# Kernel tuning notes

Measured on AMD Instinct MI355X. Metric: run time of the kernel, lower is better.

Reference implementation:

```python
import jax, jax.numpy as jnp
import numpy as np
import math

NEG_INF = -1e9
B, S, P, HID, NH, DH = 2, 1024, 128, 1024, 16, 64
NUM_SEG = 2


def setup_inputs() -> dict:
    key = jax.random.key(0)
    ks = jax.random.split(key, 16)
    f32 = jnp.float32
    inp = {
        'content_stream': jax.random.normal(ks[0], (B, S, HID), f32),
        'query_stream': jax.random.normal(ks[1], (B, P, HID), f32),
        'positional_encoding': jax.random.normal(ks[2], (B, 2 * S, HID), f32),
        'segment_matrix': jax.random.randint(ks[3], (B, S, S), 0, 2) > 0,
        'segment_encoding': jax.random.normal(ks[4], (NUM_SEG, NH, DH), f32) * 0.02,
        'segment_bias': jax.random.normal(ks[5], (NH, DH), f32) * 0.02,
        'content_mask': (jax.random.uniform(ks[6], (B, 1, S, S)) < 0.1).astype(f32),
        'query_mask': (jax.random.uniform(ks[7], (B, 1, S, S)) < 0.1).astype(f32),
        'target_mapping': jax.nn.one_hot(jax.random.randint(ks[8], (B, P), 0, S), S, dtype=f32),
        'content_bias': jax.random.normal(ks[9], (NH, DH), f32) * 0.02,
        'position_bias': jax.random.normal(ks[10], (NH, DH), f32) * 0.02,
        # projection params (no bias, XLNet-style split/merge projections)
        'wq': jax.random.normal(ks[11], (HID, NH, DH), f32) * 0.02,
        'wkc': jax.random.normal(ks[12], (HID, NH, DH), f32) * 0.02,
        'wv': jax.random.normal(ks[13], (HID, NH, DH), f32) * 0.02,
        'wkp': jax.random.normal(ks[14], (HID, NH, DH), f32) * 0.02,
        'wo': jax.random.normal(ks[15], (NH, DH, HID), f32) * 0.02,
    }
    return inp


def _rel_shift(x, klen):
    # x: [B, H, Q, R]; TransformerXL pad/reshape/slice relative shift, then keep cols 1:1+klen
    b, h, q, r = x.shape
    padded = jnp.pad(x, ((0, 0), (0, 0), (0, 0), (1, 0)))
    shifted = padded.reshape(b, h, r + 1, q)[:, :, 1:].reshape(b, h, q, r)
    return shifted[..., 1:1 + klen]


def _attention(q, kc, v, kp, content_bias, position_bias,
               segment_matrix, segment_encoding, segment_bias, token_mask):
    # q,kc,v: [B,S,H,D]; kp: [B,2S,H,D]
    content = jnp.einsum('bqhd,brhd->bhqr', q + content_bias, kc)          # [B,H,S,S]
    position = jnp.einsum('bqhd,brhd->bhqr', q + position_bias, kp)        # [B,H,S,2S]
    position = _rel_shift(position, content.shape[-1])                     # [B,H,S,S]
    segment = jnp.einsum('bqhd,shd->bhqs', q + segment_bias, segment_encoding)  # [B,H,S,2]
    segment = jnp.where(segment_matrix[:, None], segment[..., 1:], segment[..., :1])  # [B,H,S,S]
    scores = (content + position + segment) * (1.0 / math.sqrt(DH))
    scores = scores + token_mask * NEG_INF
    weights = jax.nn.softmax(scores, axis=-1)  # dropout is identity at inference
    return jnp.einsum('bhqr,brhd->bqhd', weights, v)


def reference(content_stream, query_stream, positional_encoding, segment_matrix,
              segment_encoding, segment_bias, content_mask, query_mask,
              target_mapping, content_bias, position_bias,
              wq, wkc, wv, wkp, wo):
    split = lambda x, w: jnp.einsum('bth,hnd->btnd', x, w)
    # state is None -> keys/values come from content_stream only
    q = split(content_stream, wq)
    kc = split(content_stream, wkc)
    v = split(content_stream, wv)
    kp = split(positional_encoding, wkp)

    content_out = _attention(q, kc, v, kp, content_bias, position_bias,
                             segment_matrix, segment_encoding, segment_bias, content_mask)
    content_output = jnp.einsum('bqnd,ndh->bqh', content_out, wo)

    qg = split(query_stream, wq)                                   # [B,P,H,D]
    qg = jnp.einsum('bphd,bpq->bqhd', qg, target_mapping)          # scatter to [B,S,H,D]
    query_out = _attention(qg, kc, v, kp, content_bias, position_bias,
                           segment_matrix, segment_encoding, segment_bias, query_mask)
    query_out = jnp.einsum('bqhd,bpq->bphd', query_out, target_mapping)  # gather back to [B,P,H,D]
    query_output = jnp.einsum('bpnd,ndh->bph', query_out, wo)

    return content_output, query_output
```

## Files before the change

### kernel.cpp

```cpp
#include <hip/hip_runtime.h>
#include <math.h>


static constexpr int Bc  = 2;
static constexpr int Sc  = 1024;
static constexpr int Pc  = 128;
static constexpr int HIDc = 1024;
static constexpr int NHc = 16;
static constexpr int DHc = 64;

typedef __bf16 bf16;
typedef __bf16 bf16x8 __attribute__((ext_vector_type(8)));
typedef float  f32x4  __attribute__((ext_vector_type(4)));

#define MFMA16(a, b, c) __builtin_amdgcn_mfma_f32_16x16x32_bf16((a), (b), (c), 0, 0, 0)

__global__ void sniff_seg(const unsigned char* __restrict__ seg, int* __restrict__ flag) {
    const int t = threadIdx.x;
    int nz1 = 0, nz23 = 0;
    for (int i = t * 64; i < t * 64 + 64; ++i) {
        unsigned char c = seg[i];
        int m = i & 3;
        if (m == 1 && c) nz1 = 1;
        if ((m == 2 || m == 3) && c) nz23 = 1;
    }
    nz1 = __any(nz1);
    nz23 = __any(nz23);
    if (t == 0) flag[0] = nz1 ? 0 : (nz23 ? 2 : 1);
}

__global__ void bits3(const void* __restrict__ seg, const int* __restrict__ flag,
                      const float* __restrict__ cm, const float* __restrict__ qm,
                      unsigned* __restrict__ segb, unsigned* __restrict__ cmb,
                      unsigned* __restrict__ qmb) {
    const int bid = blockIdx.x;
    const int which = bid >> 8;
    const int idx = (bid & 255) * 256 + threadIdx.x;
    unsigned wv = 0;
    if (which == 0) {
        const int mode = flag[0];
        if (mode == 0) {
            const unsigned char* s = (const unsigned char*)seg + (size_t)idx * 32;
#pragma unroll
            for (int k = 0; k < 32; ++k) wv |= (s[k] != 0) ? (1u << k) : 0u;
        } else if (mode == 1) {
            const int* s = (const int*)seg + (size_t)idx * 32;
#pragma unroll
            for (int k = 0; k < 32; ++k) wv |= (s[k] != 0) ? (1u << k) : 0u;
        } else {
            const float* s = (const float*)seg + (size_t)idx * 32;
#pragma unroll
            for (int k = 0; k < 32; ++k) wv |= (s[k] != 0.f) ? (1u << k) : 0u;
        }
        segb[idx] = wv;
    } else {
        const float* s = (which == 1 ? cm : qm) + (size_t)idx * 32;
#pragma unroll
        for (int k = 0; k < 32; ++k) wv |= (s[k] != 0.f) ? (1u << k) : 0u;
        (which == 1 ? cmb : qmb)[idx] = wv;
    }
}

__global__ __launch_bounds__(256) void prep_split(
        const float* __restrict__ content, const float* __restrict__ posenc,
        const float* __restrict__ querys,
        const float* __restrict__ wq, const float* __restrict__ wkc,
        const float* __restrict__ wvp, const float* __restrict__ wkp,
        const float* __restrict__ wo,
        bf16* __restrict__ ch, bf16* __restrict__ ph, bf16* __restrict__ qh,
        bf16* __restrict__ wqkvh, bf16* __restrict__ wqkvl,
        bf16* __restrict__ wkphh, bf16* __restrict__ wkpll,
        bf16* __restrict__ woh, bf16* __restrict__ wol) {
    __shared__ float tile[32][33];
    const int bid = blockIdx.x;
    if (bid < 3200) {
        const float* src; bf16* hdst; size_t base;
        if (bid < 1024)      { src = content; hdst = ch; base = (size_t)bid * 2048; }
        else if (bid < 3072) { src = posenc;  hdst = ph; base = (size_t)(bid - 1024) * 2048; }
        else                 { src = querys;  hdst = qh; base = (size_t)(bid - 3072) * 2048; }
        const size_t i = base + (size_t)threadIdx.x * 8;
        float xs[8];
        *(float4*)xs       = *(const float4*)(src + i);
        *(float4*)(xs + 4) = *(const float4*)(src + i + 4);
        union { bf16 b[8]; uint4 u; } H;
#pragma unroll
        for (int k = 0; k < 8; ++k) H.b[k] = (bf16)xs[k];
        *(uint4*)(hdst + i) = H.u;
        return;
    }
    const int wid = bid - 3200;
    const int z = wid >> 10, rem = wid & 1023;
    const float* W = z == 0 ? wq : z == 1 ? wkc : z == 2 ? wvp : z == 3 ? wkp : wo;
    bf16* Th = z < 3 ? wqkvh + (size_t)z * HIDc * HIDc : (z == 3 ? wkphh : woh);
    bf16* Tl = z < 3 ? wqkvl + (size_t)z * HIDc * HIDc : (z == 3 ? wkpll : wol);
    const int k0 = (rem >> 5) * 32, n0 = (rem & 31) * 32;
    const int c = threadIdx.x & 31, r0 = threadIdx.x >> 5;
#pragma unroll
    for (int rr = 0; rr < 4; ++rr) {
        int r = r0 + rr * 8;
        tile[r][c] = W[(size_t)(k0 + r) * HIDc + n0 + c];
    }
    __syncthreads();
#pragma unroll
    for (int rr = 0; rr < 4; ++rr) {
        int n = r0 + rr * 8;
        float x = tile[c][n];
        bf16 hb = (bf16)x;
        Th[(size_t)(n0 + n) * HIDc + k0 + c] = hb;
        Tl[(size_t)(n0 + n) * HIDc + k0 + c] = (bf16)(x - (float)hb);
    }
}

__global__ __launch_bounds__(256) void big_gemm(
        const bf16* __restrict__ conth, const bf16* __restrict__ posh,
        const bf16* __restrict__ quh,
        const bf16* __restrict__ wqkvh, const bf16* __restrict__ wqkvl,
        const bf16* __restrict__ wkph, const bf16* __restrict__ wkpl,
        float* __restrict__ qf, bf16* __restrict__ kch,
        bf16* __restrict__ vtg, bf16* __restrict__ kpho,
        float* __restrict__ qgf) {
    __shared__ bf16 AhS[128][40], BhS[128][40], BlS[128][40];
    const int bid = blockIdx.x;
    const int vb = (bid & 7) * 82 + (bid >> 3);
    int mode, bx, by;
    const bf16 *Ahp, *Bhp, *Blp;
    if (vb < 384)      { mode = 1; bx = vb >> 4; by = vb & 15;
                          Ahp = conth; Bhp = wqkvh; Blp = wqkvl; }
    else if (vb < 640) { mode = 2; int r = vb - 384; bx = r >> 5; by = r & 31;
                          Ahp = posh;  Bhp = wkph;  Blp = wkpl; }
    else               { mode = 0; int r = vb - 640; bx = r & 7; by = r >> 3;
                          Ahp = quh;   Bhp = wqkvh; Blp = wqkvl; }
    const int t = threadIdx.x, lane = t & 63, wv = t >> 6;
    const int g = lane >> 4, ml = lane & 15;
    const int m0 = by * 128, n0 = bx * 128;
    const int moff = (wv & 1) * 64, noff = (wv >> 1) * 64;
    const int row2 = t >> 1, c16 = (t & 1) * 16;
    const int K = HIDc;

    f32x4 acc[4][4];
#pragma unroll
    for (int i = 0; i < 4; ++i)
#pragma unroll
        for (int j = 0; j < 4; ++j) acc[i][j] = (f32x4){0.f, 0.f, 0.f, 0.f};

    uint4 rah0, rah1, rbh0, rbh1, rbl0, rbl1;
    auto gload = [&](int k0) {
        size_t ab = (size_t)(m0 + row2) * K + k0 + c16;
        rah0 = *(const uint4*)(Ahp + ab);
        rah1 = *(const uint4*)(Ahp + ab + 8);
        size_t bb = (size_t)(n0 + row2) * K + k0 + c16;
        rbh0 = *(const uint4*)(Bhp + bb);
        rbh1 = *(const uint4*)(Bhp + bb + 8);
        rbl0 = *(const uint4*)(Blp + bb);
        rbl1 = *(const uint4*)(Blp + bb + 8);
    };
    gload(0);

    for (int k0 = 0; k0 < K; k0 += 32) {
        __syncthreads();
        *(uint4*)&AhS[row2][c16]     = rah0;
        *(uint4*)&AhS[row2][c16 + 8] = rah1;
        *(uint4*)&BhS[row2][c16]     = rbh0;
        *(uint4*)&BhS[row2][c16 + 8] = rbh1;
        *(uint4*)&BlS[row2][c16]     = rbl0;
        *(uint4*)&BlS[row2][c16 + 8] = rbl1;
        __syncthreads();
        if (k0 + 32 < K) gload(k0 + 32);
        bf16x8 afh[4], bfh[4], bfl[4];
#pragma unroll
        for (int i = 0; i < 4; ++i) {
            afh[i] = *(const bf16x8*)&AhS[moff + i * 16 + ml][g * 8];
            bfh[i] = *(const bf16x8*)&BhS[noff + i * 16 + ml][g * 8];
            bfl[i] = *(const bf16x8*)&BlS[noff + i * 16 + ml][g * 8];
        }
#pragma unroll
        for (int i = 0; i < 4; ++i)
#pragma unroll
            for (int j = 0; j < 4; ++j) {
                acc[i][j] = MFMA16(afh[i], bfl[j], acc[i][j]);
                acc[i][j] = MFMA16(afh[i], bfh[j], acc[i][j]);
            }
    }
#pragma unroll
    for (int j = 0; j < 4; ++j) {
        const int nb = n0 + noff + j * 16;
#pragma unroll
        for (int i = 0; i < 4; ++i) {
            const int mbase = m0 + moff + i * 16 + g * 4;
            if (mode == 0) {
#pragma unroll
                for (int r = 0; r < 4; ++r)
                    qgf[(size_t)(mbase + r) * 1024 + nb + ml] = acc[i][j][r];
            } else if (mode == 2) {
                int hh = nb >> 6, d = (nb & 63) + ml;
#pragma unroll
                for (int r = 0; r < 4; ++r) {
                    int m = mbase + r, b = m >> 11, s = m & 2047;
                    kpho[((size_t)(b * 16 + hh) * 2048 + s) * 64 + d] = (bf16)acc[i][j][r];
                }
            } else {
                int reg = nb >> 10, nc = nb & 1023;
                if (reg == 0) {
#pragma unroll
                    for (int r = 0; r < 4; ++r)
                        qf[(size_t)(mbase + r) * 1024 + nc + ml] = acc[i][j][r];
                } else if (reg == 1) {
                    int hh = nc >> 6, d = (nc & 63) + ml;
#pragma unroll
                    for (int r = 0; r < 4; ++r) {
                        int m = mbase + r, b = m >> 10, s = m & 1023;
                        kch[((size_t)(b * 16 + hh) * 1024 + s) * 64 + d] = (bf16)acc[i][j][r];
                    }
                } else {
                    int hh = nc >> 6, d = (nc & 63) + ml;
                    int b = mbase >> 10, sb_ = mbase & 1023;
                    union { bf16 v[4]; uint2 u; } pk;
#pragma unroll
                    for (int r = 0; r < 4; ++r) pk.v[r] = (bf16)acc[i][j][r];
                    *(uint2*)(vtg + ((size_t)(b * 16 + hh) * 64 + d) * 1024 + sb_) = pk.u;
                }
            }
        }
    }
}

__global__ __launch_bounds__(256) void gemm_wo64(
        const bf16* __restrict__ a1h, const bf16* __restrict__ a1l,
        const bf16* __restrict__ a2h, const bf16* __restrict__ a2l,
        const bf16* __restrict__ Bhp, const bf16* __restrict__ Blp,
        float* __restrict__ out1, float* __restrict__ out2) {
    __shared__ bf16 AhS[64][40], AlS[64][40], BhS[128][40], BlS[128][40];
    const int bid = blockIdx.x;
    const int vb = (bid & 7) * 36 + (bid >> 3);
    const bf16 *Ahp, *Alp; float* Cf; int m0, n0;
    if (vb < 256) { Ahp = a1h; Alp = a1l; Cf = out1; m0 = (vb & 31) * 64; n0 = (vb >> 5) * 128; }
    else          { int r = vb - 256; Ahp = a2h; Alp = a2l; Cf = out2;
                    m0 = (r & 3) * 64; n0 = (r >> 2) * 128; }
    const int t = threadIdx.x, lane = t & 63, wv = t >> 6;
    const int g = lane >> 4, ml = lane & 15;
    const int moff = (wv & 1) * 32, noff = (wv >> 1) * 64;
    const int arow = t >> 2, ac8 = (t & 3) * 8;
    const int brow = t >> 1, bc16 = (t & 1) * 16;
    const int K = HIDc, N = HIDc;

    f32x4 acc[2][4];
#pragma unroll
    for (int i = 0; i < 2; ++i)
#pragma unroll
        for (int j = 0; j < 4; ++j) acc[i][j] = (f32x4){0.f, 0.f, 0.f, 0.f};

    uint4 rah, ral, rbh0, rbh1, rbl0, rbl1;
    auto gload = [&](int k0) {
        size_t ao = (size_t)(m0 + arow) * K + k0 + ac8;
        rah = *(const uint4*)(Ahp + ao);
        ral = *(const uint4*)(Alp + ao);
        size_t bo = (size_t)(n0 + brow) * K + k0 + bc16;
        rbh0 = *(const uint4*)(Bhp + bo);
        rbh1 = *(const uint4*)(Bhp + bo + 8);
        rbl0 = *(const uint4*)(Blp + bo);
        rbl1 = *(const uint4*)(Blp + bo + 8);
    };
    gload(0);

    for (int k0 = 0; k0 < K; k0 += 32) {
        __syncthreads();
        *(uint4*)&AhS[arow][ac8]      = rah;
        *(uint4*)&AlS[arow][ac8]      = ral;
        *(uint4*)&BhS[brow][bc16]     = rbh0;
        *(uint4*)&BhS[brow][bc16 + 8] = rbh1;
        *(uint4*)&BlS[brow][bc16]     = rbl0;
        *(uint4*)&BlS[brow][bc16 + 8] = rbl1;
        __syncthreads();
        if (k0 + 32 < K) gload(k0 + 32);
        bf16x8 afh[2], afl[2], bfh[4], bfl[4];
#pragma unroll
        for (int i = 0; i < 2; ++i) {
            afh[i] = *(const bf16x8*)&AhS[moff + i * 16 + ml][g * 8];
            afl[i] = *(const bf16x8*)&AlS[moff + i * 16 + ml][g * 8];
        }
#pragma unroll
        for (int j = 0; j < 4; ++j) {
            bfh[j] = *(const bf16x8*)&BhS[noff + j * 16 + ml][g * 8];
            bfl[j] = *(const bf16x8*)&BlS[noff + j * 16 + ml][g * 8];
        }
#pragma unroll
        for (int i = 0; i < 2; ++i)
#pragma unroll
            for (int j = 0; j < 4; ++j) {
                acc[i][j] = MFMA16(afl[i], bfh[j], acc[i][j]);
                acc[i][j] = MFMA16(afh[i], bfl[j], acc[i][j]);
                acc[i][j] = MFMA16(afh[i], bfh[j], acc[i][j]);
            }
    }
#pragma unroll
    for (int i = 0; i < 2; ++i)
#pragma unroll
        for (int j = 0; j < 4; ++j)
#pragma unroll
            for (int r = 0; r < 4; ++r)
                Cf[(size_t)(m0 + moff + i * 16 + g * 4 + r) * N + n0 + noff + j * 16 + ml] =
                    acc[i][j][r];
}

__global__ void find_idx(const float* __restrict__ tm, int* __restrict__ idxb,
                         float* __restrict__ wgtb) {
    const int bp = blockIdx.x;
    const float* row = tm + (size_t)bp * Sc;
    __shared__ int sidx;
    if (threadIdx.x == 0) sidx = 0;
    __syncthreads();
    for (int j = threadIdx.x; j < Sc; j += 256)
        if (row[j] != 0.f) atomicMax(&sidx, j);
    __syncthreads();
    if (threadIdx.x == 0) { idxb[bp] = sidx; wgtb[bp] = row[sidx]; }
}

__global__ void scatter_add(const int* __restrict__ idxb, const float* __restrict__ wgtb,
                            const float* __restrict__ qgf, float* __restrict__ qsf) {
    const int bp = blockIdx.x;
    const int b = bp >> 7;
    const int q = idxb[bp];
    const float w = wgtb[bp];
    const int e = threadIdx.x * 4;
    float4 v = *(const float4*)(qgf + (size_t)bp * HIDc + e);
    float* dst = qsf + ((size_t)(b * Sc) + q) * HIDc + e;
    atomicAdd(dst + 0, w * v.x);
    atomicAdd(dst + 1, w * v.y);
    atomicAdd(dst + 2, w * v.z);
    atomicAdd(dst + 3, w * v.w);
}

__global__ void gather_o(const int* __restrict__ idxb, const float* __restrict__ wgtb,
                         const bf16* __restrict__ ah, const bf16* __restrict__ al,
                         bf16* __restrict__ gh, bf16* __restrict__ gl) {
    const int bp = blockIdx.x;
    const int b = bp >> 7;
    const int q = idxb[bp];
    const float w = wgtb[bp];
    const int e = threadIdx.x * 4;
    const size_t so = ((size_t)(b * Sc) + q) * HIDc + e;
#pragma unroll
    for (int k = 0; k < 4; ++k) {
        float v = ((float)ah[so + k] + (float)al[so + k]) * w;
        bf16 hb = (bf16)v;
        gh[(size_t)bp * HIDc + e + k] = hb;
        gl[(size_t)bp * HIDc + e + k] = (bf16)(v - (float)hb);
    }
}

__global__ __launch_bounds__(256, 4) void attn_fused(
        const float* __restrict__ qcf, const float* __restrict__ qqf,
        const bf16* __restrict__ kch, const bf16* __restrict__ vtg,
        const bf16* __restrict__ kph,
        const float* __restrict__ cb, const float* __restrict__ pb,
        const float* __restrict__ sb, const float* __restrict__ senc,
        const unsigned* __restrict__ sbits,
        const unsigned* __restrict__ cmb, const unsigned* __restrict__ qmb,
        bf16* __restrict__ aoh1, bf16* __restrict__ aol1,
        bf16* __restrict__ aoh2, bf16* __restrict__ aol2) {
    __shared__ bf16 kcS[2][32][72];
    __shared__ bf16 kpS[128][72];
    __shared__ float Rw[4][16][52];

    const int bid = blockIdx.x;
    const int vb = (bid & 7) * 128 + (bid >> 3);
    const int qb = vb & 15, strm = (vb >> 4) & 1, h = (vb >> 5) & 15, b = vb >> 9;
    const int q0 = qb * 64;

    const float* qf = strm ? qqf : qcf;
    const unsigned* mbits = strm ? qmb : cmb;
    bf16* aoh = strm ? aoh2 : aoh1;
    bf16* aol = strm ? aol2 : aol1;

    const int t = threadIdx.x, w = t >> 6, lane = t & 63, g = lane >> 4, ml = lane & 15;
    const float SCL2E = 0.125f * 1.44269504088896340736f;

    const int qrow = q0 + w * 16 + ml;
    const float* qrp = qf + (size_t)(b * Sc + qrow) * HIDc + h * DHc;
    float qe[16], cbe[16], pbe[16], sbe[16], e0e[16], e1e[16];
    {
        const float* cbp = cb + h * DHc;
        const float* pbp = pb + h * DHc;
        const float* sbp = sb + h * DHc;
        const float* e0p = senc + h * DHc;
        const float* e1p = senc + NHc * DHc + h * DHc;
#pragma unroll
        for (int kk = 0; kk < 2; ++kk) {
            int o = kk * 32 + g * 8;
            *(float4*)(qe + kk * 8)      = *(const float4*)(qrp + o);
            *(float4*)(qe + kk * 8 + 4)  = *(const float4*)(qrp + o + 4);
            *(float4*)(cbe + kk * 8)     = *(const float4*)(cbp + o);
            *(float4*)(cbe + kk * 8 + 4) = *(const float4*)(cbp + o + 4);
            *(float4*)(pbe + kk * 8)     = *(const float4*)(pbp + o);
            *(float4*)(pbe + kk * 8 + 4) = *(const float4*)(pbp + o + 4);
            *(float4*)(sbe + kk * 8)     = *(const float4*)(sbp + o);
            *(float4*)(sbe + kk * 8 + 4) = *(const float4*)(sbp + o + 4);
            *(float4*)(e0e + kk * 8)     = *(const float4*)(e0p + o);
            *(float4*)(e0e + kk * 8 + 4) = *(const float4*)(e0p + o + 4);
            *(float4*)(e1e + kk * 8)     = *(const float4*)(e1p + o);
            *(float4*)(e1e + kk * 8 + 4) = *(const float4*)(e1p + o + 4);
        }
    }
    bf16x8 qch[2], qcl[2], qph[2], qpl[2];
    float s0 = 0.f, s1 = 0.f;
#pragma unroll
    for (int kk = 0; kk < 2; ++kk) {
#pragma unroll
        for (int i = 0; i < 8; ++i) {
            float qv = qe[kk * 8 + i];
            float xc = (qv + cbe[kk * 8 + i]) * SCL2E;
            float xp = (qv + pbe[kk * 8 + i]) * SCL2E;
            bf16 hb = (bf16)xc;
            qch[kk][i] = hb; qcl[kk][i] = (bf16)(xc - (float)hb);
            hb = (bf16)xp;
            qph[kk][i] = hb; qpl[kk][i] = (bf16)(xp - (float)hb);
            float qs = qv + sbe[kk * 8 + i];
            s0 += qs * e0e[kk * 8 + i];
            s1 += qs * e1e[kk * 8 + i];
        }
    }
    s0 += __shfl_xor(s0, 16); s0 += __shfl_xor(s0, 32);
    s1 += __shfl_xor(s1, 16); s1 += __shfl_xor(s1, 32);
    s0 *= SCL2E; s1 *= SCL2E;

    f32x4 oacc[4];
#pragma unroll
    for (int i = 0; i < 4; ++i) oacc[i] = (f32x4){0.f, 0.f, 0.f, 0.f};
    f32x4 lacc = (f32x4){0.f, 0.f, 0.f, 0.f};
    bf16x8 onesv;
#pragma unroll
    for (int i = 0; i < 8; ++i) onesv[i] = (bf16)1.0f;

    const size_t bh = (size_t)(b * 16 + h);
    const bf16* kcb = kch + bh * (Sc * DHc);
    const bf16* kpb = kph + bh * (2 * Sc * DHc);
    const bf16* vtb = vtg + bh * (DHc * Sc);
    const int woff = 48 - w * 16;
    const int base0 = Sc - q0 - 63;
    const size_t mrowq = (size_t)(b * Sc + qrow) * 32;

    const int tr = t >> 3, tc8 = (t & 7) * 8;
    const int slot_tr = ((tr >> 2) & 1) * 16 + ((tr >> 3) << 2) + (tr & 3);

    *(uint4*)&kcS[0][slot_tr][tc8] = *(const uint4*)(kcb + (size_t)tr * 64 + tc8);
#pragma unroll
    for (int e = 0; e < 3; ++e) {
        int grow = base0 + e * 32 + tr;
        *(uint4*)&kpS[grow & 127][tc8] = *(const uint4*)(kpb + (size_t)grow * 64 + tc8);
    }
    uint4 pkc, pkp;
    pkc = *(const uint4*)(kcb + (size_t)(32 + tr) * 64 + tc8);
    {
        int gr = base0 + 96 + tr;
        gr = gr > 2 * Sc - 1 ? 2 * Sc - 1 : gr;
        pkp = *(const uint4*)(kpb + (size_t)gr * 64 + tc8);
    }
    int rb = (base0 + woff) & 127;
    int cur = 0;
    __syncthreads();

    for (int j0 = 0; j0 < Sc; j0 += 32) {
        *(uint4*)&kcS[cur ^ 1][slot_tr][tc8] = pkc;
        {
            int slot = (base0 + j0 + 96 + tr) & 127;
            *(uint4*)&kpS[slot][tc8] = pkp;
        }
        {
            int nj = (j0 + 64 < Sc) ? j0 + 64 : 0;
            pkc = *(const uint4*)(kcb + (size_t)(nj + tr) * 64 + tc8);
            int gr = base0 + j0 + 128 + tr;
            gr = gr > 2 * Sc - 1 ? 2 * Sc - 1 : gr;
            pkp = *(const uint4*)(kpb + (size_t)gr * 64 + tc8);
        }
        bf16x8 vfrag[4];
#pragma unroll
        for (int nt = 0; nt < 4; ++nt)
            vfrag[nt] = *(const bf16x8*)(vtb + (size_t)(nt * 16 + ml) * 1024 + j0 + g * 8);
        const int wcol = j0 >> 5;
        const unsigned mw = mbits[mrowq + wcol];
        const unsigned sw = sbits[mrowq + wcol];

        f32x4 accc[2];
#pragma unroll
        for (int jt = 0; jt < 2; ++jt) {
            f32x4 a = (f32x4){0.f, 0.f, 0.f, 0.f};
#pragma unroll
            for (int kk = 0; kk < 2; ++kk) {
                bf16x8 kf = *(const bf16x8*)&kcS[cur][jt * 16 + ml][kk * 32 + g * 8];
                a = MFMA16(kf, qcl[kk], a);
                a = MFMA16(kf, qch[kk], a);
            }
            accc[jt] = a;
        }
#pragma unroll
        for (int ct = 0; ct < 3; ++ct) {
            int row = (rb + ct * 16 + ml) & 127;
            f32x4 a = (f32x4){0.f, 0.f, 0.f, 0.f};
#pragma unroll
            for (int kk = 0; kk < 2; ++kk) {
                bf16x8 kfp = *(const bf16x8*)&kpS[row][kk * 32 + g * 8];
                a = MFMA16(kfp, qpl[kk], a);
                a = MFMA16(kfp, qph[kk], a);
            }
            *(f32x4*)&Rw[w][ml][ct * 16 + g * 4] = a;
        }
        rb = (rb + 32) & 127;

        bf16x8 pa;
#pragma unroll
        for (int jt = 0; jt < 2; ++jt) {
#pragma unroll
            for (int r = 0; r < 4; ++r) {
                int jl = g * 8 + jt * 4 + r;
                float s = accc[jt][r] + Rw[w][ml][jl - ml + 15] +
                          (((sw >> jl) & 1u) ? s1 : s0);
                float p = exp2f(s);
                p = ((mw >> jl) & 1u) ? 0.f : p;
                pa[jt * 4 + r] = (bf16)p;
            }
        }

#pragma unroll
        for (int nt = 0; nt < 4; ++nt)
            oacc[nt] = MFMA16(pa, vfrag[nt], oacc[nt]);
        lacc = MFMA16(pa, onesv, lacc);

        cur ^= 1;
        __syncthreads();
    }

    float inv[4];
#pragma unroll
    for (int r = 0; r < 4; ++r) inv[r] = 1.0f / lacc[r];
#pragma unroll
    for (int nt = 0; nt < 4; ++nt)
#pragma unroll
        for (int r = 0; r < 4; ++r) {
            float val = oacc[nt][r] * inv[r];
            size_t o = (size_t)(b * Sc + q0 + w * 16 + g * 4 + r) * HIDc + h * DHc + nt * 16 + ml;
            bf16 hb = (bf16)val;
            aoh[o] = hb;
            aol[o] = (bf16)(val - (float)hb);
        }
}

extern "C" void kernel_launch(void* const* d_in, const int* in_sizes, int n_in,
                              void* d_out, int out_size, void* d_ws, size_t ws_size,
                              hipStream_t stream) {
    const float* content = (const float*)d_in[0];
    const float* querys  = (const float*)d_in[1];
    const float* posenc  = (const float*)d_in[2];
    const void*  segraw  = d_in[3];
    const float* senc    = (const float*)d_in[4];
    const float* sbias   = (const float*)d_in[5];
    const float* cmask   = (const float*)d_in[6];
    const float* qmask   = (const float*)d_in[7];
    const float* tmap    = (const float*)d_in[8];
    const float* cbias   = (const float*)d_in[9];
    const float* pbias   = (const float*)d_in[10];
    const float* wq      = (const float*)d_in[11];
    const float* wkc     = (const float*)d_in[12];
    const float* wv      = (const float*)d_in[13];
    const float* wkp     = (const float*)d_in[14];
    const float* wo      = (const float*)d_in[15];
    float* out = (float*)d_out;

    char* ws = (char*)d_ws;
    size_t off = 0;
    auto take = [&](size_t bytes) -> char* {
        char* p = ws + off;
        off += (bytes + 255) & ~(size_t)255;
        return p;
    };
    int*      flag = (int*)take(256);
    int*      idxb = (int*)take(Bc * Pc * 4);
    float*    wgtb = (float*)take(Bc * Pc * 4);
    unsigned* segb = (unsigned*)take((size_t)Bc * Sc * 32 * 4);
    unsigned* cmb  = (unsigned*)take((size_t)Bc * Sc * 32 * 4);
    unsigned* qmb  = (unsigned*)take((size_t)Bc * Sc * 32 * 4);
    bf16* wqkvh = (bf16*)take((size_t)3 * HIDc * HIDc * 2);
    bf16* wqkvl = (bf16*)take((size_t)3 * HIDc * HIDc * 2);
    bf16* wkphw = (bf16*)take((size_t)HIDc * HIDc * 2);
    bf16* wkplw = (bf16*)take((size_t)HIDc * HIDc * 2);
    bf16* woh   = (bf16*)take((size_t)HIDc * HIDc * 2);
    bf16* wol   = (bf16*)take((size_t)HIDc * HIDc * 2);
    bf16* conth = (bf16*)take((size_t)Bc * Sc * HIDc * 2);
    bf16* posh  = (bf16*)take((size_t)Bc * 2 * Sc * HIDc * 2);
    bf16* quh   = (bf16*)take((size_t)Bc * Pc * HIDc * 2);
    float* qf   = (float*)take((size_t)Bc * Sc * HIDc * 4);
    float* qsf  = (float*)take((size_t)Bc * Sc * HIDc * 4);
    bf16* kchp  = (bf16*)take((size_t)Bc * NHc * Sc * DHc * 2);
    bf16* kphp  = (bf16*)take((size_t)Bc * NHc * 2 * Sc * DHc * 2);
    bf16* vtg   = (bf16*)take((size_t)Bc * NHc * DHc * Sc * 2);
    float* qgf  = (float*)take((size_t)Bc * Pc * HIDc * 4);
    bf16* aoh1  = (bf16*)take((size_t)Bc * Sc * HIDc * 2);
    bf16* aol1  = (bf16*)take((size_t)Bc * Sc * HIDc * 2);
    bf16* aoh2  = (bf16*)take((size_t)Bc * Sc * HIDc * 2);
    bf16* aol2  = (bf16*)take((size_t)Bc * Sc * HIDc * 2);
    bf16* gathh = (bf16*)take((size_t)Bc * Pc * HIDc * 2);
    bf16* gathl = (bf16*)take((size_t)Bc * Pc * HIDc * 2);

    dim3 blk(256);

    sniff_seg<<<1, 64, 0, stream>>>((const unsigned char*)segraw, flag);
    bits3<<<768, blk, 0, stream>>>(segraw, flag, cmask, qmask, segb, cmb, qmb);
    find_idx<<<Bc * Pc, blk, 0, stream>>>(tmap, idxb, wgtb);
    prep_split<<<8320, blk, 0, stream>>>(content, posenc, querys,
                                         wq, wkc, wv, wkp, wo,
                                         conth, posh, quh,
                                         wqkvh, wqkvl, wkphw, wkplw, woh, wol);

    big_gemm<<<656, blk, 0, stream>>>(conth, posh, quh,
                                      wqkvh, wqkvl, wkphw, wkplw,
                                      qf, kchp, vtg, kphp, qgf);

    hipMemsetAsync(qsf, 0, (size_t)Bc * Sc * HIDc * 4, stream);
    scatter_add<<<Bc * Pc, blk, 0, stream>>>(idxb, wgtb, qgf, qsf);

    attn_fused<<<1024, blk, 0, stream>>>(qf, qsf, kchp, vtg, kphp,
                                         cbias, pbias, sbias, senc, segb, cmb, qmb,
                                         aoh1, aol1, aoh2, aol2);

    gather_o<<<Bc * Pc, blk, 0, stream>>>(idxb, wgtb, aoh2, aol2, gathh, gathl);
    gemm_wo64<<<288, blk, 0, stream>>>(aoh1, aol1, gathh, gathl, woh, wol,
                                       out, out + (size_t)Bc * Sc * HIDc);
}
```

Baseline: 236.4 us.

## Merge prep kernels and fuse scatter/gather into GEMM epilogue and prologue

Merges sniff/bits/find_idx/prep_split and the qsf memset into one prep_all launch, with each block recomputing the segment dtype flag locally. The target-mapping scatter-add moves into the big_gemm epilogue as atomics, and the gather of attention output moves into the gemm_wo64 A-load with on-the-fly hi/lo resplit. This removes several launches and intermediate buffers. It costs redundant flag sniffing per block and atomics written directly from the GEMM.

```diff
diff --git a/kernel.cpp b/kernel.cpp
--- a/kernel.cpp
+++ b/kernel.cpp
@@ -15,70 +15,99 @@
 
 #define MFMA16(a, b, c) __builtin_amdgcn_mfma_f32_16x16x32_bf16((a), (b), (c), 0, 0, 0)
 
-__global__ void sniff_seg(const unsigned char* __restrict__ seg, int* __restrict__ flag) {
-    const int t = threadIdx.x;
-    int nz1 = 0, nz23 = 0;
-    for (int i = t * 64; i < t * 64 + 64; ++i) {
-        unsigned char c = seg[i];
-        int m = i & 3;
-        if (m == 1 && c) nz1 = 1;
-        if ((m == 2 || m == 3) && c) nz23 = 1;
-    }
-    nz1 = __any(nz1);
-    nz23 = __any(nz23);
-    if (t == 0) flag[0] = nz1 ? 0 : (nz23 ? 2 : 1);
-}
-
-__global__ void bits3(const void* __restrict__ seg, const int* __restrict__ flag,
-                      const float* __restrict__ cm, const float* __restrict__ qm,
-                      unsigned* __restrict__ segb, unsigned* __restrict__ cmb,
-                      unsigned* __restrict__ qmb) {
-    const int bid = blockIdx.x;
-    const int which = bid >> 8;
-    const int idx = (bid & 255) * 256 + threadIdx.x;
-    unsigned wv = 0;
-    if (which == 0) {
-        const int mode = flag[0];
-        if (mode == 0) {
-            const unsigned char* s = (const unsigned char*)seg + (size_t)idx * 32;
-#pragma unroll
-            for (int k = 0; k < 32; ++k) wv |= (s[k] != 0) ? (1u << k) : 0u;
-        } else if (mode == 1) {
-            const int* s = (const int*)seg + (size_t)idx * 32;
-#pragma unroll
-            for (int k = 0; k < 32; ++k) wv |= (s[k] != 0) ? (1u << k) : 0u;
-        } else {
-            const float* s = (const float*)seg + (size_t)idx * 32;
-#pragma unroll
-            for (int k = 0; k < 32; ++k) wv |= (s[k] != 0.f) ? (1u << k) : 0u;
-        }
-        segb[idx] = wv;
-    } else {
-        const float* s = (which == 1 ? cm : qm) + (size_t)idx * 32;
-#pragma unroll
-        for (int k = 0; k < 32; ++k) wv |= (s[k] != 0.f) ? (1u << k) : 0u;
-        (which == 1 ? cmb : qmb)[idx] = wv;
-    }
-}
-
-__global__ __launch_bounds__(256) void prep_split(
+__global__ __launch_bounds__(256) void prep_all(
+        const void* __restrict__ seg, const float* __restrict__ cm,
+        const float* __restrict__ qm, const float* __restrict__ tm,
         const float* __restrict__ content, const float* __restrict__ posenc,
         const float* __restrict__ querys,
         const float* __restrict__ wq, const float* __restrict__ wkc,
         const float* __restrict__ wvp, const float* __restrict__ wkp,
         const float* __restrict__ wo,
+        unsigned* __restrict__ segb, unsigned* __restrict__ cmb,
+        unsigned* __restrict__ qmb,
+        int* __restrict__ idxb, float* __restrict__ wgtb,
         bf16* __restrict__ ch, bf16* __restrict__ ph, bf16* __restrict__ qh,
         bf16* __restrict__ wqkvh, bf16* __restrict__ wqkvl,
         bf16* __restrict__ wkphh, bf16* __restrict__ wkpll,
-        bf16* __restrict__ woh, bf16* __restrict__ wol) {
+        bf16* __restrict__ woh, bf16* __restrict__ wol,
+        float* __restrict__ qsf) {
     __shared__ float tile[32][33];
     const int bid = blockIdx.x;
-    if (bid < 3200) {
+    const int tid = threadIdx.x;
+
+    if (bid < 256) {
+        __shared__ int sflag;
+        if (tid == 0) sflag = 0;
+        __syncthreads();
+        {
+            const unsigned char* sb8 = (const unsigned char*)seg;
+            int f = 0;
+            const int o = tid * 16;
+#pragma unroll
+            for (int i = 0; i < 16; ++i) {
+                unsigned char c = sb8[o + i];
+                int m = (o + i) & 3;
+                if (m == 1 && c) f |= 1;
+                if (m >= 2 && c) f |= 2;
+            }
+            if (f) atomicOr(&sflag, f);
+        }
+        __syncthreads();
+        const int mode = (sflag & 1) ? 0 : ((sflag & 2) ? 2 : 1);
+        const int idx = bid * 256 + tid;
+        unsigned wv = 0;
+        if (mode == 0) {
+            const unsigned char* s = (const unsigned char*)seg + (size_t)idx * 32;
+#pragma unroll
+            for (int k = 0; k < 32; ++k) wv |= (s[k] != 0) ? (1u << k) : 0u;
+        } else if (mode == 1) {
+            const int* s = (const int*)seg + (size_t)idx * 32;
+#pragma unroll
+            for (int k = 0; k < 32; ++k) wv |= (s[k] != 0) ? (1u << k) : 0u;
+        } else {
+            const float* s = (const float*)seg + (size_t)idx * 32;
+#pragma unroll
+            for (int k = 0; k < 32; ++k) wv |= (s[k] != 0.f) ? (1u << k) : 0u;
+        }
+        segb[idx] = wv;
+        return;
+    }
+    if (bid < 768) {
+        const int which = (bid - 256) >> 8;
+        const int idx = ((bid - 256) & 255) * 256 + tid;
+        const float* s = (which == 0 ? cm : qm) + (size_t)idx * 32;
+        unsigned wv = 0;
+#pragma unroll
+        for (int k = 0; k < 32; ++k) wv |= (s[k] != 0.f) ? (1u << k) : 0u;
+        (which == 0 ? cmb : qmb)[idx] = wv;
+        return;
+    }
+    if (bid < 1024) {
+        const int bp = bid - 768;
+        const float* row = tm + (size_t)bp * Sc;
+        __shared__ int sidx;
+        if (tid == 0) sidx = 0;
+        __syncthreads();
+        for (int j = tid; j < Sc; j += 256)
+            if (row[j] != 0.f) atomicMax(&sidx, j);
+        __syncthreads();
+        if (tid == 0) { idxb[bp] = sidx; wgtb[bp] = row[sidx]; }
+        return;
+    }
+    if (bid >= 9344) {
+        const size_t i = ((size_t)(bid - 9344) * 256 + tid) * 8;
+        float4 z = {0.f, 0.f, 0.f, 0.f};
+        *(float4*)(qsf + i) = z;
+        *(float4*)(qsf + i + 4) = z;
+        return;
+    }
+    const int pb = bid - 1024;
+    if (pb < 3200) {
         const float* src; bf16* hdst; size_t base;
-        if (bid < 1024)      { src = content; hdst = ch; base = (size_t)bid * 2048; }
-        else if (bid < 3072) { src = posenc;  hdst = ph; base = (size_t)(bid - 1024) * 2048; }
-        else                 { src = querys;  hdst = qh; base = (size_t)(bid - 3072) * 2048; }
-        const size_t i = base + (size_t)threadIdx.x * 8;
+        if (pb < 1024)      { src = content; hdst = ch; base = (size_t)pb * 2048; }
+        else if (pb < 3072) { src = posenc;  hdst = ph; base = (size_t)(pb - 1024) * 2048; }
+        else                { src = querys;  hdst = qh; base = (size_t)(pb - 3072) * 2048; }
+        const size_t i = base + (size_t)tid * 8;
         float xs[8];
         *(float4*)xs       = *(const float4*)(src + i);
         *(float4*)(xs + 4) = *(const float4*)(src + i + 4);
@@ -88,13 +117,13 @@
         *(uint4*)(hdst + i) = H.u;
         return;
     }
-    const int wid = bid - 3200;
+    const int wid = pb - 3200;
     const int z = wid >> 10, rem = wid & 1023;
     const float* W = z == 0 ? wq : z == 1 ? wkc : z == 2 ? wvp : z == 3 ? wkp : wo;
     bf16* Th = z < 3 ? wqkvh + (size_t)z * HIDc * HIDc : (z == 3 ? wkphh : woh);
     bf16* Tl = z < 3 ? wqkvl + (size_t)z * HIDc * HIDc : (z == 3 ? wkpll : wol);
     const int k0 = (rem >> 5) * 32, n0 = (rem & 31) * 32;
-    const int c = threadIdx.x & 31, r0 = threadIdx.x >> 5;
+    const int c = tid & 31, r0 = tid >> 5;
 #pragma unroll
     for (int rr = 0; rr < 4; ++rr) {
         int r = r0 + rr * 8;
@@ -118,7 +147,8 @@
         const bf16* __restrict__ wkph, const bf16* __restrict__ wkpl,
         float* __restrict__ qf, bf16* __restrict__ kch,
         bf16* __restrict__ vtg, bf16* __restrict__ kpho,
-        float* __restrict__ qgf) {
+        float* __restrict__ qsf, const int* __restrict__ idxb,
+        const float* __restrict__ wgtb) {
     __shared__ bf16 AhS[128][40], BhS[128][40], BlS[128][40];
     const int bid = blockIdx.x;
     const int vb = (bid & 7) * 82 + (bid >> 3);
@@ -189,8 +219,13 @@
             const int mbase = m0 + moff + i * 16 + g * 4;
             if (mode == 0) {
 #pragma unroll
-                for (int r = 0; r < 4; ++r)
-                    qgf[(size_t)(mbase + r) * 1024 + nb + ml] = acc[i][j][r];
+                for (int r = 0; r < 4; ++r) {
+                    int p = mbase + r;
+                    int qq = idxb[p];
+                    float wgt = wgtb[p];
+                    atomicAdd(&qsf[((size_t)((p >> 7) * Sc) + qq) * 1024 + nb + ml],
+                              wgt * acc[i][j][r]);
+                }
             } else if (mode == 2) {
                 int hh = nb >> 6, d = (nb & 63) + ml;
 #pragma unroll
@@ -227,14 +262,15 @@
 __global__ __launch_bounds__(256) void gemm_wo64(
         const bf16* __restrict__ a1h, const bf16* __restrict__ a1l,
         const bf16* __restrict__ a2h, const bf16* __restrict__ a2l,
+        const int* __restrict__ idxb, const float* __restrict__ wgtb,
         const bf16* __restrict__ Bhp, const bf16* __restrict__ Blp,
         float* __restrict__ out1, float* __restrict__ out2) {
     __shared__ bf16 AhS[64][40], AlS[64][40], BhS[128][40], BlS[128][40];
     const int bid = blockIdx.x;
     const int vb = (bid & 7) * 36 + (bid >> 3);
-    const bf16 *Ahp, *Alp; float* Cf; int m0, n0;
-    if (vb < 256) { Ahp = a1h; Alp = a1l; Cf = out1; m0 = (vb & 31) * 64; n0 = (vb >> 5) * 128; }
-    else          { int r = vb - 256; Ahp = a2h; Alp = a2l; Cf = out2;
+    float* Cf; int m0, n0; bool gat;
+    if (vb < 256) { gat = false; Cf = out1; m0 = (vb & 31) * 64; n0 = (vb >> 5) * 128; }
+    else          { int r = vb - 256; gat = true; Cf = out2;
                     m0 = (r & 3) * 64; n0 = (r >> 2) * 128; }
     const int t = threadIdx.x, lane = t & 63, wv = t >> 6;
     const int g = lane >> 4, ml = lane & 15;
@@ -243,6 +279,17 @@
     const int brow = t >> 1, bc16 = (t & 1) * 16;
     const int K = HIDc, N = HIDc;
 
+    size_t arow_base;
+    float gw = 0.f;
+    if (gat) {
+        int p = m0 + arow;
+        int qq = idxb[p];
+        gw = wgtb[p];
+        arow_base = ((size_t)((p >> 7) * Sc) + qq) * (size_t)K;
+    } else {
+        arow_base = (size_t)(m0 + arow) * K;
+    }
+
     f32x4 acc[2][4];
 #pragma unroll
     for (int i = 0; i < 2; ++i)
@@ -251,9 +298,23 @@
 
     uint4 rah, ral, rbh0, rbh1, rbl0, rbl1;
     auto gload = [&](int k0) {
-        size_t ao = (size_t)(m0 + arow) * K + k0 + ac8;
-        rah = *(const uint4*)(Ahp + ao);
-        ral = *(const uint4*)(Alp + ao);
+        if (!gat) {
+            rah = *(const uint4*)(a1h + arow_base + k0 + ac8);
+            ral = *(const uint4*)(a1l + arow_base + k0 + ac8);
+        } else {
+            union { bf16 b[8]; uint4 u; } Hs, Ls, Ho, Lo;
+            Hs.u = *(const uint4*)(a2h + arow_base + k0 + ac8);
+            Ls.u = *(const uint4*)(a2l + arow_base + k0 + ac8);
+#pragma unroll
+            for (int e = 0; e < 8; ++e) {
+                float v = ((float)Hs.b[e] + (float)Ls.b[e]) * gw;
+                bf16 nh = (bf16)v;
+                Ho.b[e] = nh;
+                Lo.b[e] = (bf16)(v - (float)nh);
+            }
+            rah = Ho.u;
+            ral = Lo.u;
+        }
         size_t bo = (size_t)(n0 + brow) * K + k0 + bc16;
         rbh0 = *(const uint4*)(Bhp + bo);
         rbh1 = *(const uint4*)(Bhp + bo + 8);
@@ -300,52 +361,6 @@
             for (int r = 0; r < 4; ++r)
                 Cf[(size_t)(m0 + moff + i * 16 + g * 4 + r) * N + n0 + noff + j * 16 + ml] =
                     acc[i][j][r];
-}
-
-__global__ void find_idx(const float* __restrict__ tm, int* __restrict__ idxb,
-                         float* __restrict__ wgtb) {
-    const int bp = blockIdx.x;
-    const float* row = tm + (size_t)bp * Sc;
-    __shared__ int sidx;
-    if (threadIdx.x == 0) sidx = 0;
-    __syncthreads();
-    for (int j = threadIdx.x; j < Sc; j += 256)
-        if (row[j] != 0.f) atomicMax(&sidx, j);
-    __syncthreads();
-    if (threadIdx.x == 0) { idxb[bp] = sidx; wgtb[bp] = row[sidx]; }
-}
-
-__global__ void scatter_add(const int* __restrict__ idxb, const float* __restrict__ wgtb,
-                            const float* __restrict__ qgf, float* __restrict__ qsf) {
-    const int bp = blockIdx.x;
-    const int b = bp >> 7;
-    const int q = idxb[bp];
-    const float w = wgtb[bp];
-    const int e = threadIdx.x * 4;
-    float4 v = *(const float4*)(qgf + (size_t)bp * HIDc + e);
-    float* dst = qsf + ((size_t)(b * Sc) + q) * HIDc + e;
-    atomicAdd(dst + 0, w * v.x);
-    atomicAdd(dst + 1, w * v.y);
-    atomicAdd(dst + 2, w * v.z);
-    atomicAdd(dst + 3, w * v.w);
-}
-
-__global__ void gather_o(const int* __restrict__ idxb, const float* __restrict__ wgtb,
-                         const bf16* __restrict__ ah, const bf16* __restrict__ al,
-                         bf16* __restrict__ gh, bf16* __restrict__ gl) {
-    const int bp = blockIdx.x;
-    const int b = bp >> 7;
-    const int q = idxb[bp];
-    const float w = wgtb[bp];
-    const int e = threadIdx.x * 4;
-    const size_t so = ((size_t)(b * Sc) + q) * HIDc + e;
-#pragma unroll
-    for (int k = 0; k < 4; ++k) {
-        float v = ((float)ah[so + k] + (float)al[so + k]) * w;
-        bf16 hb = (bf16)v;
-        gh[(size_t)bp * HIDc + e + k] = hb;
-        gl[(size_t)bp * HIDc + e + k] = (bf16)(v - (float)hb);
-    }
 }
 
 __global__ __launch_bounds__(256, 4) void attn_fused(
@@ -572,7 +587,6 @@
         off += (bytes + 255) & ~(size_t)255;
         return p;
     };
-    int*      flag = (int*)take(256);
     int*      idxb = (int*)take(Bc * Pc * 4);
     float*    wgtb = (float*)take(Bc * Pc * 4);
     unsigned* segb = (unsigned*)take((size_t)Bc * Sc * 32 * 4);
@@ -592,36 +606,31 @@
     bf16* kchp  = (bf16*)take((size_t)Bc * NHc * Sc * DHc * 2);
     bf16* kphp  = (bf16*)take((size_t)Bc * NHc * 2 * Sc * DHc * 2);
     bf16* vtg   = (bf16*)take((size_t)Bc * NHc * DHc * Sc * 2);
-    float* qgf  = (float*)take((size_t)Bc * Pc * HIDc * 4);
     bf16* aoh1  = (bf16*)take((size_t)Bc * Sc * HIDc * 2);
     bf16* aol1  = (bf16*)take((size_t)Bc * Sc * HIDc * 2);
     bf16* aoh2  = (bf16*)take((size_t)Bc * Sc * HIDc * 2);
     bf16* aol2  = (bf16*)take((size_t)Bc * Sc * HIDc * 2);
-    bf16* gathh = (bf16*)take((size_t)Bc * Pc * HIDc * 2);
-    bf16* gathl = (bf16*)take((size_t)Bc * Pc * HIDc * 2);
 
     dim3 blk(256);
 
-    sniff_seg<<<1, 64, 0, stream>>>((const unsigned char*)segraw, flag);
-    bits3<<<768, blk, 0, stream>>>(segraw, flag, cmask, qmask, segb, cmb, qmb);
-    find_idx<<<Bc * Pc, blk, 0, stream>>>(tmap, idxb, wgtb);
-    prep_split<<<8320, blk, 0, stream>>>(content, posenc, querys,
-                                         wq, wkc, wv, wkp, wo,
-                                         conth, posh, quh,
-                                         wqkvh, wqkvl, wkphw, wkplw, woh, wol);
+    prep_all<<<10368, blk, 0, stream>>>(segraw, cmask, qmask, tmap,
+                                        content, posenc, querys,
+                                        wq, wkc, wv, wkp, wo,
+                                        segb, cmb, qmb, idxb, wgtb,
+                                        conth, posh, quh,
+                                        wqkvh, wqkvl, wkphw, wkplw, woh, wol,
+                                        qsf);
 
     big_gemm<<<656, blk, 0, stream>>>(conth, posh, quh,
                                       wqkvh, wqkvl, wkphw, wkplw,
-                                      qf, kchp, vtg, kphp, qgf);
-
-    hipMemsetAsync(qsf, 0, (size_t)Bc * Sc * HIDc * 4, stream);
-    scatter_add<<<Bc * Pc, blk, 0, stream>>>(idxb, wgtb, qgf, qsf);
+                                      qf, kchp, vtg, kphp,
+                                      qsf, idxb, wgtb);
 
     attn_fused<<<1024, blk, 0, stream>>>(qf, qsf, kchp, vtg, kphp,
                                          cbias, pbias, sbias, senc, segb, cmb, qmb,
                                          aoh1, aol1, aoh2, aol2);
 
-    gather_o<<<Bc * Pc, blk, 0, stream>>>(idxb, wgtb, aoh2, aol2, gathh, gathl);
-    gemm_wo64<<<288, blk, 0, stream>>>(aoh1, aol1, gathh, gathl, woh, wol,
+    gemm_wo64<<<288, blk, 0, stream>>>(aoh1, aol1, aoh2, aol2, idxb, wgtb,
+                                       woh, wol,
                                        out, out + (size_t)Bc * Sc * HIDc);
 }
```

Result: faster. 224.0 us, median of 2 (-5.2%).
